# Optimization experiments

Measured on AMD Instinct MI355X. Metric: run time of the kernel, lower is better.

The kernel has to match this reference:

```python
import jax, jax.numpy as jnp
import numpy as np
from jax import lax

D_MODEL = 64
D_STATE = 128
D_INNER = 128  # d_model * expand_factor; must equal D_STATE for the original code to broadcast
BATCH = 4
SEQ = 1024
LN_EPS = 1e-5


def setup_inputs() -> dict:
    key = jax.random.key(0)
    ks = jax.random.split(key, 12)
    s = 0.05
    return {
        "x": jax.random.normal(ks[0], (BATCH, SEQ, D_MODEL), jnp.float32),
        "W_in": jax.random.normal(ks[1], (2 * D_INNER, D_MODEL), jnp.float32) * s,
        "W_delta": jax.random.normal(ks[2], (D_INNER, D_MODEL), jnp.float32) * s,
        "b_delta": jax.random.normal(ks[3], (D_INNER,), jnp.float32) * s,
        "W_B": jax.random.normal(ks[4], (D_STATE, D_MODEL), jnp.float32) * s,
        "b_B": jax.random.normal(ks[5], (D_STATE,), jnp.float32) * s,
        "W_C": jax.random.normal(ks[6], (D_STATE, D_MODEL), jnp.float32) * s,
        "b_C": jax.random.normal(ks[7], (D_STATE,), jnp.float32) * s,
        "A": jax.random.normal(ks[8], (D_INNER, D_STATE), jnp.float32) * 0.01,
        "W_out": jax.random.normal(ks[9], (D_MODEL, D_INNER), jnp.float32) * s,
        "ln_w": jnp.ones((D_MODEL,), jnp.float32),
        "ln_b": jnp.zeros((D_MODEL,), jnp.float32),
    }


def _layer_norm(x, w, b):
    mu = x.mean(-1, keepdims=True)
    var = ((x - mu) ** 2).mean(-1, keepdims=True)
    return (x - mu) * lax.rsqrt(var + LN_EPS) * w + b


def reference(x, W_in, W_delta, b_delta, W_B, b_B, W_C, b_C, A, W_out, ln_w, ln_b):
    # projections
    xp = jnp.einsum('bld,ed->ble', x, W_in)            # (B, L, 2*d_inner)
    x_ssm, gate = xp[..., :D_INNER], xp[..., D_INNER:]
    delta = jax.nn.softplus(jnp.einsum('bld,id->bli', x, W_delta) + b_delta)  # (B, L, d_inner)
    Bm = jnp.einsum('bld,sd->bls', x, W_B) + b_B        # (B, L, d_state)
    Cm = jnp.einsum('bld,sd->bls', x, W_C) + b_C        # (B, L, d_state)

    # A_discrete.mean(dim=1): mean over d_inner of exp(delta * A)
    Abar = jnp.exp(delta[..., :, None] * A).mean(axis=2)  # (B, L, d_state)
    x_pool = x_ssm.mean(axis=-1)                          # (B, L) mean over d_inner
    Bx = Bm * x_pool[..., None]                           # (B, L, d_state)

    def step(h, inp):
        a_t, bx_t, c_t = inp                              # each (B, d_state)
        h = a_t * h + bx_t
        y = (c_t * h).sum(axis=-1)                        # (B,)
        return h, y

    h0 = jnp.zeros((x.shape[0], D_STATE), x.dtype)
    _, ys = lax.scan(step, h0,
                     (jnp.swapaxes(Abar, 0, 1), jnp.swapaxes(Bx, 0, 1), jnp.swapaxes(Cm, 0, 1)))
    y = jnp.swapaxes(ys, 0, 1)[..., None]                 # (B, L, 1) -> broadcast over d_inner

    y = y * jax.nn.silu(gate)                             # (B, L, d_inner)
    out = jnp.einsum('bli,di->bld', y, W_out)             # (B, L, d_model)
    return _layer_norm(out + x, ln_w, ln_b)
```

## Files before the change

### kernel.cpp

```cpp
#include <hip/hip_runtime.h>
#include <math.h>

#define NB   4
#define SL   1024
#define NTOK (NB*SL)
#define DM   64
#define DI   128
#define DSt  128
#define SEGLEN 8
#define NSEG (SL/SEGLEN)
#define NSEG_ALL (NB*NSEG)

#define OFF_GATE   0
#define OFF_DELTA  (OFF_GATE  + NTOK*DI)
#define OFF_BM     (OFF_DELTA + NTOK*DI)
#define OFF_CM     (OFF_BM    + NTOK*DSt)
#define OFF_XPOOL  (OFF_CM    + NTOK*DSt)
#define OFF_ABAR   (OFF_XPOOL + NTOK)
#define OFF_HEND   (OFF_ABAR  + NTOK*DSt)
#define OFF_P      (OFF_HEND  + NSEG_ALL*DSt)
#define OFF_W4     (OFF_P     + NSEG_ALL*DSt)

#define PROJ_TOK 16
#define PROJ_TG  (NTOK/PROJ_TOK)

static __device__ __forceinline__ float wave64_sum(float v) {
#pragma unroll
    for (int m = 32; m >= 1; m >>= 1) v += __shfl_xor(v, m, 64);
    return v;
}

static __device__ __forceinline__ float fast_exp2(float x) {
    float r;
    asm("v_exp_f32 %0, %1" : "=v"(r) : "v"(x));
    return r;
}

static __device__ __forceinline__ float softplus_f(float x) {
    return fmaxf(x, 0.f) + __logf(1.f + __expf(-fabsf(x)));
}

static __device__ __forceinline__ void pin4(float4& v) {
    asm volatile("" : "+v"(v.x), "+v"(v.y), "+v"(v.z), "+v"(v.w));
}

#if __has_builtin(__builtin_amdgcn_global_load_lds)
#define HAVE_GLL 1
static __device__ __forceinline__ void gload_lds16(const float4* g, float4* l) {
    __builtin_amdgcn_global_load_lds(
        (const __attribute__((address_space(1))) void*)g,
        (__attribute__((address_space(3))) void*)l,
        16, 0, 0);
}
#else
#define HAVE_GLL 0
#endif

__global__ __launch_bounds__(256, 2) void k_proj(
    const float* __restrict__ x, const float* __restrict__ W_in,
    const float* __restrict__ W_delta, const float* __restrict__ b_delta,
    const float* __restrict__ W_B, const float* __restrict__ b_B,
    const float* __restrict__ W_C, const float* __restrict__ b_C,
    const float* __restrict__ W_out, float* __restrict__ ws)
{
    __shared__ float4 Wl[DI*16];
    const int tid = threadIdx.x;

    if (blockIdx.x == 4*PROJ_TG) {
        const float4* Wg = (const float4*)W_out;
        float4* W4 = (float4*)(ws + OFF_W4);
#pragma unroll
        for (int j = 0; j < 8; ++j) {
            const int f = tid + j*256;
            const int d = f >> 5, q = f & 31;
            W4[q*64 + d] = Wg[f];
        }
        return;
    }

    const int l   = tid & 63;
    const int w   = tid >> 6;
    const int cat = blockIdx.x >> 8;
    const int tg  = blockIdx.x & 255;
    const int tok0 = tg * PROJ_TOK;

    const float* Wbase; const float* bias; float* dst;
    if      (cat == 0) { Wbase = W_in + DI*DM; bias = nullptr; dst = ws + OFF_GATE;  }
    else if (cat == 1) { Wbase = W_delta;      bias = b_delta; dst = ws + OFF_DELTA; }
    else if (cat == 2) { Wbase = W_B;          bias = b_B;     dst = ws + OFF_BM;    }
    else               { Wbase = W_C;          bias = b_C;     dst = ws + OFF_CM;    }

    {
        const float4* Wg = (const float4*)Wbase;
#if HAVE_GLL
#pragma unroll
        for (int j = 0; j < 8; ++j) {
            const int f   = tid + j*256;
            const int row = f >> 4, kk = f & 15;
            const int src = row*16 + (kk ^ (row & 15));
            gload_lds16(Wg + src, Wl + f);
        }
#else
#pragma unroll
        for (int j = 0; j < 8; ++j) {
            const int f = tid + j*256;
            const int row = f >> 4, k = f & 15;
            Wl[row*16 + (k ^ (row & 15))] = Wg[f];
        }
#endif
    }
    __syncthreads();

    float4 w0[16], w1[16];
#pragma unroll
    for (int k = 0; k < 16; ++k) {
        w0[k] = Wl[l*16      + (k ^ (l & 15))];
        w1[k] = Wl[(l+64)*16 + (k ^ (l & 15))];
    }
#pragma unroll
    for (int k = 0; k < 16; ++k) { pin4(w0[k]); pin4(w1[k]); }

    float bias0 = 0.f, bias1 = 0.f;
    if (bias) { bias0 = bias[l]; bias1 = bias[l+64]; }

#pragma unroll
    for (int it = 0; it < PROJ_TOK/4; ++it) {
        const int tlu = __builtin_amdgcn_readfirstlane(it*4 + w);
        const float4* xt = (const float4*)(x + (tok0 + tlu)*DM);
        float a0=0.f,a1=0.f,a2=0.f,a3=0.f, c0=0.f,c1=0.f,c2=0.f,c3=0.f;
#pragma unroll
        for (int k = 0; k < 16; ++k) {
            const float4 xv = xt[k];
            a0 = fmaf(w0[k].x, xv.x, a0);
            a1 = fmaf(w0[k].y, xv.y, a1);
            a2 = fmaf(w0[k].z, xv.z, a2);
            a3 = fmaf(w0[k].w, xv.w, a3);
            c0 = fmaf(w1[k].x, xv.x, c0);
            c1 = fmaf(w1[k].y, xv.y, c1);
            c2 = fmaf(w1[k].z, xv.z, c2);
            c3 = fmaf(w1[k].w, xv.w, c3);
        }
        float ra = (a0+a1) + (a2+a3) + bias0;
        float rb = (c0+c1) + (c2+c3) + bias1;
        if (cat == 1) { ra = softplus_f(ra); rb = softplus_f(rb); }
        const int tok = tok0 + tlu;
        dst[tok*128 + l]      = ra;
        dst[tok*128 + 64 + l] = rb;
    }

    if (cat == 0) {
        float wp = 0.f;
#pragma unroll 8
        for (int i = 0; i < DI; ++i) wp += W_in[i*DM + l];
        wp *= (1.0f/DI);
#pragma unroll
        for (int it = 0; it < PROJ_TOK/4; ++it) {
            const int tl = it*4 + w;
            float v = x[(tok0 + tl)*DM + l] * wp;
            v = wave64_sum(v);
            if (l == 0) ws[OFF_XPOOL + tok0 + tl] = v;
        }
    }
}

__global__ __launch_bounds__(256) void k_abar_scan1(const float* __restrict__ A,
                                                    float* __restrict__ ws)
{
    __shared__ float psum[4][SEGLEN][64];
    __shared__ float abL[SEGLEN][64];
    const int tid  = threadIdx.x;
    const int lane = tid & 63;
    const int igrp = tid >> 6;
    const int g    = blockIdx.x >> 1;
    const int sh   = blockIdx.x & 1;
    const int s    = sh*64 + lane;
    const int t0   = g * SEGLEN;

    float areg[32];
#pragma unroll
    for (int i = 0; i < 32; ++i)
        areg[i] = A[(igrp*32 + i)*DSt + s] * 1.44269504f;

    const float* delta = ws + OFF_DELTA;
    float*       Abar  = ws + OFF_ABAR;

#pragma unroll
    for (int t = 0; t < SEGLEN; ++t) {
        const float* dv = delta + (t0 + t)*DI + igrp*32;
        float a0=0.f,a1=0.f,a2=0.f,a3=0.f;
#pragma unroll
        for (int q = 0; q < 8; ++q) {
            const float4 d4 = *(const float4*)(dv + 4*q);
            a0 += fast_exp2(d4.x * areg[4*q    ]);
            a1 += fast_exp2(d4.y * areg[4*q + 1]);
            a2 += fast_exp2(d4.z * areg[4*q + 2]);
            a3 += fast_exp2(d4.w * areg[4*q + 3]);
        }
        psum[igrp][t][lane] = (a0+a1) + (a2+a3);
    }
    __syncthreads();

#pragma unroll
    for (int it = tid; it < SEGLEN*64; it += 256) {
        const int t = it >> 6, l2 = it & 63;
        float v = (psum[0][t][l2] + psum[1][t][l2])
                + (psum[2][t][l2] + psum[3][t][l2]);
        v *= (1.0f/DI);
        abL[t][l2] = v;
        Abar[(t0 + t)*DSt + sh*64 + l2] = v;
    }
    __syncthreads();

    if (tid < 64) {
        const float* Bm    = ws + OFF_BM;
        const float* xpool = ws + OFF_XPOOL;
        float bx[SEGLEN];
#pragma unroll
        for (int t = 0; t < SEGLEN; ++t)
            bx[t] = Bm[(t0 + t)*DSt + s] * xpool[t0 + t];
        float h = 0.f, pr = 1.f;
#pragma unroll
        for (int t = 0; t < SEGLEN; ++t) {
            const float a = abL[t][lane];
            h = fmaf(a, h, bx[t]);
            pr *= a;
        }
        ws[OFF_HEND + g*DSt + s] = h;
        ws[OFF_P    + g*DSt + s] = pr;
    }
}

__global__ __launch_bounds__(256) void k_tail(
    const float* __restrict__ x, const float* __restrict__ ln_w,
    const float* __restrict__ ln_b, const float* __restrict__ ws,
    float* __restrict__ out)
{
    __shared__ float prod[SEGLEN][132];
    __shared__ float y_lds[SEGLEN];
    __shared__ float vall[SEGLEN][DI];
    __shared__ float psum[4][SEGLEN][64];

    const int tid = threadIdx.x;
    const int b   = blockIdx.x >> 7;
    const int seg = blockIdx.x & 127;
    const int t0  = b*SL + seg*SEGLEN;
    const int d   = tid & 63;
    const int wv  = tid >> 6;

    const float* gate = ws + OFF_GATE;
    const float4* W4  = (const float4*)(ws + OFF_W4);
    float gv[4];
#pragma unroll
    for (int j = 0; j < 4; ++j) {
        const int idx = j*256 + tid;
        const int tl = idx >> 7, dd = idx & 127;
        gv[j] = gate[(t0 + tl)*DI + dd];
    }
    float4 wq[8];
#pragma unroll
    for (int j = 0; j < 8; ++j)
        wq[j] = W4[(wv*8 + j)*64 + d];
    float xres[2];
#pragma unroll
    for (int jt = 0; jt < 2; ++jt)
        xres[jt] = x[(t0 + wv*2 + jt)*DM + d];
    const float lw = ln_w[d], lb = ln_b[d];

    if (tid < 128) {
        const int s = tid;
        const float* Abar  = ws + OFF_ABAR;
        const float* Bm    = ws + OFF_BM;
        const float* Cm    = ws + OFF_CM;
        const float* xpool = ws + OFF_XPOOL;
        const float* hend  = ws + OFF_HEND;
        const float* P     = ws + OFF_P;

        float aA[SEGLEN], aB[SEGLEN], aC[SEGLEN];
#pragma unroll
        for (int t = 0; t < SEGLEN; ++t) {
            aA[t] = Abar[(t0 + t)*DSt + s];
            aB[t] = Bm[(t0 + t)*DSt + s] * xpool[t0 + t];
            aC[t] = Cm[(t0 + t)*DSt + s];
        }
        float h = 0.f;
#pragma unroll 8
        for (int j = 0; j < seg; ++j) {
            const int idx = (b*NSEG + j)*DSt + s;
            h = fmaf(P[idx], h, hend[idx]);
        }
#pragma unroll
        for (int t = 0; t < SEGLEN; ++t) {
            h = fmaf(aA[t], h, aB[t]);
            prod[t][s] = aC[t] * h;
        }
    }
    __syncthreads();

    if (tid < 128) {
        const int t = tid >> 4, r = tid & 15;
        float4 u0 = *(const float4*)(&prod[t][r*8]);
        float4 u1 = *(const float4*)(&prod[t][r*8 + 4]);
        float acc = ((u0.x+u0.y) + (u0.z+u0.w)) + ((u1.x+u1.y) + (u1.z+u1.w));
#pragma unroll
        for (int m = 1; m <= 8; m <<= 1) acc += __shfl_xor(acc, m, 64);
        if (r == 0) y_lds[t] = acc;
    }
    __syncthreads();

#pragma unroll
    for (int j = 0; j < 4; ++j) {
        const int idx = j*256 + tid;
        const int tl = idx >> 7, dd = idx & 127;
        const float g = gv[j];
        vall[tl][dd] = y_lds[tl] * (g / (1.f + __expf(-g)));
    }
    __syncthreads();

    float ac[8];
#pragma unroll
    for (int t = 0; t < 8; ++t) ac[t] = 0.f;
#pragma unroll
    for (int j = 0; j < 8; ++j) {
        const float4 w4 = wq[j];
#pragma unroll
        for (int t = 0; t < 8; ++t) {
            const float4 v = *(const float4*)(&vall[t][(wv*8 + j)*4]);
            ac[t] = fmaf(w4.x, v.x, ac[t]);
            ac[t] = fmaf(w4.y, v.y, ac[t]);
            ac[t] = fmaf(w4.z, v.z, ac[t]);
            ac[t] = fmaf(w4.w, v.w, ac[t]);
        }
    }
#pragma unroll
    for (int t = 0; t < 8; ++t) psum[wv][t][d] = ac[t];
    __syncthreads();

#pragma unroll
    for (int jt = 0; jt < 2; ++jt) {
        const int tl  = wv*2 + jt;
        const int tok = t0 + tl;
        const float z = ((psum[0][tl][d] + psum[1][tl][d])
                       + (psum[2][tl][d] + psum[3][tl][d])) + xres[jt];
        const float s1 = wave64_sum(z);
        const float s2 = wave64_sum(z*z);
        const float mu  = s1 * (1.f/64.f);
        const float var = s2 * (1.f/64.f) - mu*mu;
        out[tok*DM + d] = (z - mu) * rsqrtf(var + 1e-5f) * lw + lb;
    }
}

extern "C" void kernel_launch(void* const* d_in, const int* in_sizes, int n_in,
                              void* d_out, int out_size, void* d_ws, size_t ws_size,
                              hipStream_t stream) {
    const float* x       = (const float*)d_in[0];
    const float* W_in    = (const float*)d_in[1];
    const float* W_delta = (const float*)d_in[2];
    const float* b_delta = (const float*)d_in[3];
    const float* W_B     = (const float*)d_in[4];
    const float* b_B     = (const float*)d_in[5];
    const float* W_C     = (const float*)d_in[6];
    const float* b_C     = (const float*)d_in[7];
    const float* A       = (const float*)d_in[8];
    const float* W_out   = (const float*)d_in[9];
    const float* ln_w    = (const float*)d_in[10];
    const float* ln_b    = (const float*)d_in[11];
    float* out = (float*)d_out;
    float* ws  = (float*)d_ws;

    hipLaunchKernelGGL(k_proj, dim3(4*PROJ_TG + 1), dim3(256), 0, stream,
                       x, W_in, W_delta, b_delta, W_B, b_B, W_C, b_C, W_out, ws);
    hipLaunchKernelGGL(k_abar_scan1, dim3(2*NSEG_ALL), dim3(256), 0, stream, A, ws);
    hipLaunchKernelGGL(k_tail,       dim3(NSEG_ALL),   dim3(256), 0, stream,
                       x, ln_w, ln_b, ws, out);
}
```

Before: 43.83 us.

## Fuse Abar/segment scan with tail using cross-block flag synchronization

Merges the Abar/segment-scan kernel and the tail kernel into one kernel with 512 blocks. Each block publishes its segment end-state and product, then sets a release flag. Later blocks spin on the flags of earlier segments before combining the carry-in, so Abar stays in LDS and is never written to the workspace. This removes one kernel launch and the global round trip of Abar/Bm. In exchange it relies on all 512 blocks being co-resident or scheduled in order, since a later block that waits without its predecessors running could deadlock.

Result: slower. 127.3 us (+190.5%).

```diff
diff --git a/kernel.cpp b/kernel.cpp
--- a/kernel.cpp
+++ b/kernel.cpp
@@ -16,10 +16,10 @@
 #define OFF_BM     (OFF_DELTA + NTOK*DI)
 #define OFF_CM     (OFF_BM    + NTOK*DSt)
 #define OFF_XPOOL  (OFF_CM    + NTOK*DSt)
-#define OFF_ABAR   (OFF_XPOOL + NTOK)
-#define OFF_HEND   (OFF_ABAR  + NTOK*DSt)
+#define OFF_HEND   (OFF_XPOOL + NTOK)
 #define OFF_P      (OFF_HEND  + NSEG_ALL*DSt)
 #define OFF_W4     (OFF_P     + NSEG_ALL*DSt)
+#define OFF_FLAG   (OFF_W4    + 8192)
 
 #define PROJ_TOK 16
 #define PROJ_TG  (NTOK/PROJ_TOK)
@@ -75,6 +75,9 @@
             const int d = f >> 5, q = f & 31;
             W4[q*64 + d] = Wg[f];
         }
+        int* flags = (int*)(ws + OFF_FLAG);
+        flags[tid]       = 0;
+        flags[tid + 256] = 0;
         return;
     }
 
@@ -163,92 +166,98 @@
     }
 }
 
-__global__ __launch_bounds__(256) void k_abar_scan1(const float* __restrict__ A,
-                                                    float* __restrict__ ws)
+__global__ __launch_bounds__(256, 2) void k_scan_tail(
+    const float* __restrict__ x, const float* __restrict__ A,
+    const float* __restrict__ ln_w, const float* __restrict__ ln_b,
+    float* __restrict__ ws, float* __restrict__ out)
 {
     __shared__ float psum[4][SEGLEN][64];
-    __shared__ float abL[SEGLEN][64];
+    __shared__ float abL[SEGLEN][DSt];
+    __shared__ float prod[SEGLEN][132];
+    __shared__ float y_lds[SEGLEN];
+    __shared__ float vall[SEGLEN][DI];
+
     const int tid  = threadIdx.x;
+    const int g    = blockIdx.x;
+    const int b    = g >> 7;
+    const int seg  = g & 127;
+    const int t0   = g * SEGLEN;
     const int lane = tid & 63;
     const int igrp = tid >> 6;
-    const int g    = blockIdx.x >> 1;
-    const int sh   = blockIdx.x & 1;
-    const int s    = sh*64 + lane;
-    const int t0   = g * SEGLEN;
-
-    float areg[32];
-#pragma unroll
-    for (int i = 0; i < 32; ++i)
-        areg[i] = A[(igrp*32 + i)*DSt + s] * 1.44269504f;
 
     const float* delta = ws + OFF_DELTA;
-    float*       Abar  = ws + OFF_ABAR;
-
-#pragma unroll
-    for (int t = 0; t < SEGLEN; ++t) {
-        const float* dv = delta + (t0 + t)*DI + igrp*32;
-        float a0=0.f,a1=0.f,a2=0.f,a3=0.f;
-#pragma unroll
-        for (int q = 0; q < 8; ++q) {
-            const float4 d4 = *(const float4*)(dv + 4*q);
-            a0 += fast_exp2(d4.x * areg[4*q    ]);
-            a1 += fast_exp2(d4.y * areg[4*q + 1]);
-            a2 += fast_exp2(d4.z * areg[4*q + 2]);
-            a3 += fast_exp2(d4.w * areg[4*q + 3]);
-        }
-        psum[igrp][t][lane] = (a0+a1) + (a2+a3);
-    }
-    __syncthreads();
-
-#pragma unroll
-    for (int it = tid; it < SEGLEN*64; it += 256) {
-        const int t = it >> 6, l2 = it & 63;
-        float v = (psum[0][t][l2] + psum[1][t][l2])
-                + (psum[2][t][l2] + psum[3][t][l2]);
-        v *= (1.0f/DI);
-        abL[t][l2] = v;
-        Abar[(t0 + t)*DSt + sh*64 + l2] = v;
-    }
-    __syncthreads();
-
-    if (tid < 64) {
-        const float* Bm    = ws + OFF_BM;
-        const float* xpool = ws + OFF_XPOOL;
-        float bx[SEGLEN];
+    const float* Bm    = ws + OFF_BM;
+    const float* Cm    = ws + OFF_CM;
+    const float* xpool = ws + OFF_XPOOL;
+    float* hend = ws + OFF_HEND;
+    float* P    = ws + OFF_P;
+    int*   flags = (int*)(ws + OFF_FLAG);
+
+#pragma unroll 1
+    for (int u = 0; u < 2; ++u) {
+        const int s = u*64 + lane;
+        float areg[32];
+#pragma unroll
+        for (int i = 0; i < 32; ++i)
+            areg[i] = A[(igrp*32 + i)*DSt + s] * 1.44269504f;
+        if (u) __syncthreads();
+#pragma unroll
+        for (int t = 0; t < SEGLEN; ++t) {
+            const float* dv = delta + (t0 + t)*DI + igrp*32;
+            float a0=0.f,a1=0.f,a2=0.f,a3=0.f;
+#pragma unroll
+            for (int q = 0; q < 8; ++q) {
+                const float4 d4 = *(const float4*)(dv + 4*q);
+                a0 += fast_exp2(d4.x * areg[4*q    ]);
+                a1 += fast_exp2(d4.y * areg[4*q + 1]);
+                a2 += fast_exp2(d4.z * areg[4*q + 2]);
+                a3 += fast_exp2(d4.w * areg[4*q + 3]);
+            }
+            psum[igrp][t][lane] = (a0+a1) + (a2+a3);
+        }
+        __syncthreads();
+#pragma unroll
+        for (int it = tid; it < SEGLEN*64; it += 256) {
+            const int t = it >> 6, l2 = it & 63;
+            float v = (psum[0][t][l2] + psum[1][t][l2])
+                    + (psum[2][t][l2] + psum[3][t][l2]);
+            abL[t][u*64 + l2] = v * (1.0f/DI);
+        }
+    }
+    __syncthreads();
+
+    float bx[SEGLEN], aC[SEGLEN];
+    if (tid < 128) {
+        const int s = tid;
 #pragma unroll
         for (int t = 0; t < SEGLEN; ++t)
             bx[t] = Bm[(t0 + t)*DSt + s] * xpool[t0 + t];
         float h = 0.f, pr = 1.f;
 #pragma unroll
         for (int t = 0; t < SEGLEN; ++t) {
-            const float a = abL[t][lane];
+            const float a = abL[t][s];
             h = fmaf(a, h, bx[t]);
             pr *= a;
         }
-        ws[OFF_HEND + g*DSt + s] = h;
-        ws[OFF_P    + g*DSt + s] = pr;
-    }
-}
-
-__global__ __launch_bounds__(256) void k_tail(
-    const float* __restrict__ x, const float* __restrict__ ln_w,
-    const float* __restrict__ ln_b, const float* __restrict__ ws,
-    float* __restrict__ out)
-{
-    __shared__ float prod[SEGLEN][132];
-    __shared__ float y_lds[SEGLEN];
-    __shared__ float vall[SEGLEN][DI];
-    __shared__ float psum[4][SEGLEN][64];
-
-    const int tid = threadIdx.x;
-    const int b   = blockIdx.x >> 7;
-    const int seg = blockIdx.x & 127;
-    const int t0  = b*SL + seg*SEGLEN;
-    const int d   = tid & 63;
-    const int wv  = tid >> 6;
+        hend[g*DSt + s] = h;
+        P[g*DSt + s]    = pr;
+#pragma unroll
+        for (int t = 0; t < SEGLEN; ++t)
+            aC[t] = Cm[(t0 + t)*DSt + s];
+    }
+    __threadfence();
+    __syncthreads();
+    if (tid == 0)
+        __hip_atomic_store(flags + g, 1, __ATOMIC_RELEASE, __HIP_MEMORY_SCOPE_AGENT);
 
     const float* gate = ws + OFF_GATE;
     const float4* W4  = (const float4*)(ws + OFF_W4);
+    const int d  = tid & 63;
+    const int wv = tid >> 6;
+    float4 wq[8];
+#pragma unroll
+    for (int j = 0; j < 8; ++j)
+        wq[j] = W4[(wv*8 + j)*64 + d];
     float gv[4];
 #pragma unroll
     for (int j = 0; j < 4; ++j) {
@@ -256,32 +265,21 @@
         const int tl = idx >> 7, dd = idx & 127;
         gv[j] = gate[(t0 + tl)*DI + dd];
     }
-    float4 wq[8];
-#pragma unroll
-    for (int j = 0; j < 8; ++j)
-        wq[j] = W4[(wv*8 + j)*64 + d];
     float xres[2];
 #pragma unroll
     for (int jt = 0; jt < 2; ++jt)
         xres[jt] = x[(t0 + wv*2 + jt)*DM + d];
     const float lw = ln_w[d], lb = ln_b[d];
 
+    if (tid < seg) {
+        while (__hip_atomic_load(flags + b*NSEG + tid,
+                                 __ATOMIC_ACQUIRE, __HIP_MEMORY_SCOPE_AGENT) == 0) {}
+    }
+    __syncthreads();
+    __threadfence();
+
     if (tid < 128) {
         const int s = tid;
-        const float* Abar  = ws + OFF_ABAR;
-        const float* Bm    = ws + OFF_BM;
-        const float* Cm    = ws + OFF_CM;
-        const float* xpool = ws + OFF_XPOOL;
-        const float* hend  = ws + OFF_HEND;
-        const float* P     = ws + OFF_P;
-
-        float aA[SEGLEN], aB[SEGLEN], aC[SEGLEN];
-#pragma unroll
-        for (int t = 0; t < SEGLEN; ++t) {
-            aA[t] = Abar[(t0 + t)*DSt + s];
-            aB[t] = Bm[(t0 + t)*DSt + s] * xpool[t0 + t];
-            aC[t] = Cm[(t0 + t)*DSt + s];
-        }
         float h = 0.f;
 #pragma unroll 8
         for (int j = 0; j < seg; ++j) {
@@ -290,7 +288,7 @@
         }
 #pragma unroll
         for (int t = 0; t < SEGLEN; ++t) {
-            h = fmaf(aA[t], h, aB[t]);
+            h = fmaf(abL[t][s], h, bx[t]);
             prod[t][s] = aC[t] * h;
         }
     }
@@ -311,8 +309,8 @@
     for (int j = 0; j < 4; ++j) {
         const int idx = j*256 + tid;
         const int tl = idx >> 7, dd = idx & 127;
-        const float g = gv[j];
-        vall[tl][dd] = y_lds[tl] * (g / (1.f + __expf(-g)));
+        const float gg = gv[j];
+        vall[tl][dd] = y_lds[tl] * (gg / (1.f + __expf(-gg)));
     }
     __syncthreads();
 
@@ -369,7 +367,6 @@
 
     hipLaunchKernelGGL(k_proj, dim3(4*PROJ_TG + 1), dim3(256), 0, stream,
                        x, W_in, W_delta, b_delta, W_B, b_B, W_C, b_C, W_out, ws);
-    hipLaunchKernelGGL(k_abar_scan1, dim3(2*NSEG_ALL), dim3(256), 0, stream, A, ws);
-    hipLaunchKernelGGL(k_tail,       dim3(NSEG_ALL),   dim3(256), 0, stream,
-                       x, ln_w, ln_b, ws, out);
-}
+    hipLaunchKernelGGL(k_scan_tail, dim3(NSEG_ALL), dim3(256), 0, stream,
+                       x, A, ln_w, ln_b, ws, out);
+}
```
